# Performance work log

Hardware: AMD Instinct MI355X
Metric: run time of the kernel (lower is better)

## Reference

```python
import jax, jax.numpy as jnp
import numpy as np

NV, NC, E = 100000, 50000, 800000   # var nodes, config nodes, edges per direction
K = 100                              # configs per graph (uniform -> static dense batch)
B = NC // K                          # number of graphs
DV, DC, DH, DO = 64, 16, 128, 64     # var feat, config feat, hidden, out


def _w(key, i, o):
    # kaiming_normal_ init as in _init_weights
    return jax.random.normal(key, (i, o), jnp.float32) * np.float32(np.sqrt(2.0 / i))


def setup_inputs() -> dict:
    key = jax.random.key(0)
    ks = jax.random.split(key, 16)
    return {
        "x_var": jax.random.normal(ks[0], (NV, DV), jnp.float32),
        "x_config": jax.random.normal(ks[1], (NC, DC), jnp.float32),
        "src_v2c": jax.random.randint(ks[2], (E,), 0, NV, jnp.int32),
        "dst_v2c": jax.random.randint(ks[3], (E,), 0, NC, jnp.int32),
        "src_c2v": jax.random.randint(ks[4], (E,), 0, NC, jnp.int32),
        "dst_c2v": jax.random.randint(ks[5], (E,), 0, NV, jnp.int32),
        "batch_config": jnp.arange(NC, dtype=jnp.int32) // K,
        # layer 1 SAGEConv params per edge type (lin_l has bias, lin_r has none)
        "Wl1_v2c": _w(ks[6], DV, DH), "bl1_v2c": jnp.zeros((DH,), jnp.float32), "Wr1_v2c": _w(ks[7], DC, DH),
        "Wl1_c2v": _w(ks[8], DC, DH), "bl1_c2v": jnp.zeros((DH,), jnp.float32), "Wr1_c2v": _w(ks[9], DV, DH),
        # layer 2 (output layer, jk=None -> maps to out_channels)
        "Wl2_v2c": _w(ks[10], DH, DO), "bl2_v2c": jnp.zeros((DO,), jnp.float32), "Wr2_v2c": _w(ks[11], DH, DO),
    }


def _sage(x_src, x_dst, src, dst, Wl, bl, Wr, n_dst):
    # PyG SAGEConv: lin_l(mean_{j in N(i)} x_src[j]) + lin_r(x_dst[i])
    msum = jax.ops.segment_sum(x_src[src], dst, num_segments=n_dst)            # [n_dst, d_src]
    cnt = jax.ops.segment_sum(jnp.ones(src.shape, x_src.dtype), dst, num_segments=n_dst)
    mean = msum / jnp.maximum(cnt, 1.0)[:, None]
    return mean @ Wl + bl + x_dst @ Wr


def reference(x_var, x_config, src_v2c, dst_v2c, src_c2v, dst_c2v, batch_config,
              Wl1_v2c, bl1_v2c, Wr1_v2c, Wl1_c2v, bl1_c2v, Wr1_c2v,
              Wl2_v2c, bl2_v2c, Wr2_v2c):
    # --- layer 1 (to_hetero: each node type updated by its incoming edge type), ReLU between layers ---
    h_config = jax.nn.relu(_sage(x_var, x_config, src_v2c, dst_v2c, Wl1_v2c, bl1_v2c, Wr1_v2c, NC))
    h_var = jax.nn.relu(_sage(x_config, x_var, src_c2v, dst_c2v, Wl1_c2v, bl1_c2v, Wr1_c2v, NV))
    # --- layer 2: only the 'config' output is consumed downstream ---
    o_config = _sage(h_var, h_config, src_v2c, dst_v2c, Wl2_v2c, bl2_v2c, Wr2_v2c, NC)  # [NC, DO]
    # --- to_dense_batch(x['config'], batch) -> [B, K, DO]; squeeze() is a no-op (no size-1 dims) ---
    cnt = jax.ops.segment_sum(jnp.ones((NC,), jnp.int32), batch_config, num_segments=B)
    starts = jnp.cumsum(cnt) - cnt
    pos = jnp.arange(NC, dtype=jnp.int32) - starts[batch_config]
    dense = jnp.zeros((B, K, DO), o_config.dtype).at[batch_config, pos].set(o_config)
    return dense
```

## Files before the change

### kernel.cpp

```cpp
#include <hip/hip_runtime.h>


#define CHUNK 4096
#define EPT 16
#define MAXBINS 1024

__global__ __launch_bounds__(256) void part_count2_kernel(
    const int* __restrict__ dstC, const int* __restrict__ dstV, int E, int nblocks,
    int nbinsC, int nbinsV, int* __restrict__ countsC, int* __restrict__ countsV) {
    const int* dst; int shift, nbins; int* counts; int b;
    if (blockIdx.x < (unsigned)nblocks) { dst = dstC; shift = 6; nbins = nbinsC; counts = countsC; b = blockIdx.x; }
    else { dst = dstV; shift = 7; nbins = nbinsV; counts = countsV; b = blockIdx.x - nblocks; }
    __shared__ int hist[MAXBINS];
    int t = threadIdx.x;
    for (int j = t; j < nbins; j += 256) hist[j] = 0;
    __syncthreads();
    int base = b * CHUNK;
#pragma unroll
    for (int j = 0; j < EPT; ++j) {
        int e = base + j * 256 + t;
        if (e < E) atomicAdd(&hist[dst[e] >> shift], 1);
    }
    __syncthreads();
    for (int j = t; j < nbins; j += 256) counts[(size_t)j * nblocks + b] = hist[j];
}

__global__ __launch_bounds__(256) void part_rowscan2_kernel(
    int* __restrict__ countsC, int nbinsC, int* __restrict__ binTotC,
    int* __restrict__ countsV, int* __restrict__ binTotV, int nblocks) {
    int* counts; int* binTot; int bin;
    if (blockIdx.x < (unsigned)nbinsC) { counts = countsC; binTot = binTotC; bin = blockIdx.x; }
    else { counts = countsV; binTot = binTotV; bin = blockIdx.x - nbinsC; }
    __shared__ int s[256];
    int t = threadIdx.x;
    int v = (t < nblocks) ? counts[(size_t)bin * nblocks + t] : 0;
    s[t] = v; __syncthreads();
    for (int o = 1; o < 256; o <<= 1) {
        int add = (t >= o) ? s[t - o] : 0; __syncthreads();
        s[t] += add; __syncthreads();
    }
    if (t < nblocks) counts[(size_t)bin * nblocks + t] = s[t] - v;
    if (t == nblocks - 1) binTot[bin] = s[t];
}

__global__ __launch_bounds__(256) void part_binscan2_kernel(
    const int* __restrict__ binTotC, int nbinsC, int* __restrict__ binBaseC,
    const int* __restrict__ binTotV, int nbinsV, int* __restrict__ binBaseV) {
    const int* binTot; int nbins; int* binBase;
    if (blockIdx.x == 0) { binTot = binTotC; nbins = nbinsC; binBase = binBaseC; }
    else { binTot = binTotV; nbins = nbinsV; binBase = binBaseV; }
    __shared__ int s[256];
    __shared__ int carry;
    int t = threadIdx.x;
    if (t == 0) carry = 0;
    __syncthreads();
    for (int c0 = 0; c0 < nbins; c0 += 256) {
        int v = (c0 + t < nbins) ? binTot[c0 + t] : 0;
        s[t] = v; __syncthreads();
        for (int o = 1; o < 256; o <<= 1) {
            int add = (t >= o) ? s[t - o] : 0; __syncthreads();
            s[t] += add; __syncthreads();
        }
        if (c0 + t < nbins) binBase[c0 + t] = carry + s[t] - v;
        __syncthreads();
        if (t == 255) carry += s[255];
        __syncthreads();
    }
    if (t == 0) binBase[nbins] = carry;
}

__global__ __launch_bounds__(256) void part_scatter2_kernel(
    const int* __restrict__ srcC, const int* __restrict__ dstC,
    const int* __restrict__ srcV, const int* __restrict__ dstV, int E, int nblocks,
    int nbinsC, const int* __restrict__ countsC, const int* __restrict__ binBaseC,
    int* __restrict__ ebufC,
    int nbinsV, const int* __restrict__ countsV, const int* __restrict__ binBaseV,
    int* __restrict__ ebufV) {
    const int *src, *dst, *counts, *binBase; int* ebuf; int shift, mask, nbins; int b;
    if (blockIdx.x < (unsigned)nblocks) {
        src = srcC; dst = dstC; counts = countsC; binBase = binBaseC; ebuf = ebufC;
        shift = 6; mask = 63; nbins = nbinsC; b = blockIdx.x;
    } else {
        src = srcV; dst = dstV; counts = countsV; binBase = binBaseV; ebuf = ebufV;
        shift = 7; mask = 127; nbins = nbinsV; b = blockIdx.x - nblocks;
    }
    __shared__ int hist[MAXBINS];
    int t = threadIdx.x;
    for (int j = t; j < nbins; j += 256) hist[j] = 0;
    __syncthreads();
    int base = b * CHUNK;
#pragma unroll
    for (int j = 0; j < EPT; ++j) {
        int e = base + j * 256 + t;
        if (e < E) {
            int d = dst[e];
            int bin = d >> shift;
            int rank = atomicAdd(&hist[bin], 1);
            int slot = binBase[bin] + counts[(size_t)bin * nblocks + b] + rank;
            ebuf[slot] = (src[e] << shift) | (d & mask);
        }
    }
}

__global__ __launch_bounds__(256) void csr2_kernel(
    int nbinsC, const int* __restrict__ binBaseC, const int* __restrict__ ebufC,
    int* __restrict__ ebufC2, int* __restrict__ offC, int nC,
    const int* __restrict__ binBaseV, const int* __restrict__ ebufV,
    int* __restrict__ ebufV2, int* __restrict__ offV, int nV, int E) {
    __shared__ int hist[128];
    __shared__ int cur[128];
    __shared__ int s[256];
    int t = threadIdx.x;
    const int *binBase, *eb1; int *eb2, *off; int n, shift, bin;
    if (blockIdx.x < (unsigned)nbinsC) {
        bin = blockIdx.x; binBase = binBaseC; eb1 = ebufC; eb2 = ebufC2; off = offC; n = nC; shift = 6;
    } else {
        bin = blockIdx.x - nbinsC; binBase = binBaseV; eb1 = ebufV; eb2 = ebufV2; off = offV; n = nV; shift = 7;
    }
    int mask = (1 << shift) - 1, nloc = 1 << shift;
    if (blockIdx.x == 0 && t == 0) { offC[nC] = E; offV[nV] = E; }
    int e0 = binBase[bin], e1 = binBase[bin + 1];
    if (t < nloc) { hist[t] = 0; cur[t] = 0; }
    __syncthreads();
    for (int e = e0 + t; e < e1; e += 256) atomicAdd(&hist[eb1[e] & mask], 1);
    __syncthreads();
    int v = (t < nloc) ? hist[t] : 0;
    s[t] = v; __syncthreads();
    for (int o = 1; o < 256; o <<= 1) {
        int add = (t >= o) ? s[t - o] : 0; __syncthreads();
        s[t] += add; __syncthreads();
    }
    if (t < nloc) {
        int node = (bin << shift) + t;
        if (node < n) off[node] = e0 + s[t] - v;
        hist[t] = s[t] - v;
    }
    __syncthreads();
    for (int e = e0 + t; e < e1; e += 256) {
        int w = eb1[e];
        int local = w & mask;
        int r = atomicAdd(&cur[local], 1);
        eb2[e0 + hist[local] + r] = w >> shift;
    }
}

__device__ __forceinline__ void gather64_body(
    const int* __restrict__ off, const int* __restrict__ eb,
    const float* __restrict__ X, float* __restrict__ M,
    const float* __restrict__ P, float* __restrict__ out,
    int n, int b, int nblocks) {
    int lane = threadIdx.x & 63, wid = threadIdx.x >> 6;
    int nw = nblocks * 4;
    for (int i = b * 4 + wid; i < n; i += nw) {
        int e0 = off[i], e1 = off[i + 1];
        int deg = e1 - e0;
        float acc = 0.f;
        for (int j0 = 0; j0 < deg; j0 += 64) {
            int m = min(deg - j0, 64);
            int idx = 0;
            if (lane < m) idx = eb[e0 + j0 + lane];
            int j = 0;
            for (; j + 4 <= m; j += 4) {
                int s0 = __shfl(idx, j);
                int s1 = __shfl(idx, j + 1);
                int s2 = __shfl(idx, j + 2);
                int s3 = __shfl(idx, j + 3);
                acc += X[(size_t)s0 * 64 + lane];
                acc += X[(size_t)s1 * 64 + lane];
                acc += X[(size_t)s2 * 64 + lane];
                acc += X[(size_t)s3 * 64 + lane];
            }
            for (; j < m; ++j) {
                int s = __shfl(idx, j);
                acc += X[(size_t)s * 64 + lane];
            }
        }
        float r = acc / fmaxf((float)deg, 1.0f);
        if (out) out[(size_t)i * 64 + lane] = r + P[(size_t)i * 64 + lane];
        else     M[(size_t)i * 64 + lane] = r;
    }
}

__device__ __forceinline__ void gather16_body(
    const int* __restrict__ off, const int* __restrict__ eb,
    const float* __restrict__ X, float* __restrict__ M, int n, int b, int nblocks) {
    int lane = threadIdx.x & 63, wid = threadIdx.x >> 6;
    int dlane = lane & 15, eg = lane >> 4;
    int nw = nblocks * 4;
    for (int i = b * 4 + wid; i < n; i += nw) {
        int e0 = off[i], e1 = off[i + 1];
        int deg = e1 - e0;
        float acc = 0.f;
        for (int j0 = 0; j0 < deg; j0 += 64) {
            int m = min(deg - j0, 64);
            int idx = 0;
            if (lane < m) idx = eb[e0 + j0 + lane];
            for (int j = eg; j < m; j += 4) {
                int s = __shfl(idx, j);
                acc += X[(size_t)s * 16 + dlane];
            }
        }
        acc += __shfl_xor(acc, 16);
        acc += __shfl_xor(acc, 32);
        if (lane < 16) M[(size_t)i * 16 + lane] = acc / fmaxf((float)deg, 1.0f);
    }
}

__global__ __launch_bounds__(256) void gather2_kernel(
    const int* __restrict__ offC, const int* __restrict__ ebC,
    const float* __restrict__ Xc, float* __restrict__ Mc, int nC, int gbC,
    const int* __restrict__ offV, const int* __restrict__ ebV,
    const float* __restrict__ Xv, float* __restrict__ Mv, int nV, int gbV) {
    if (blockIdx.x < (unsigned)gbC)
        gather64_body(offC, ebC, Xc, Mc, nullptr, nullptr, nC, blockIdx.x, gbC);
    else
        gather16_body(offV, ebV, Xv, Mv, nV, blockIdx.x - gbC, gbV);
}

__global__ __launch_bounds__(256) void gather64_add_kernel(
    const int* __restrict__ off, const int* __restrict__ eb,
    const float* __restrict__ X, const float* __restrict__ P,
    float* __restrict__ out, int n) {
    gather64_body(off, eb, X, nullptr, P, out, n, blockIdx.x, gridDim.x);
}

template<int D, int ROW0>
__device__ __forceinline__ void stageF_swz(const float* __restrict__ A, float* __restrict__ Fb,
                                           int i0, int n, int t) {
    const int Q = D / 4;
    const int NPP = 256 / Q;
#pragma unroll
    for (int p = 0; p < 64 / NPP; ++p) {
        int nn = t / Q + p * NPP;
        int k4 = t % Q;
        int node = i0 + nn;
        float4 v = make_float4(0.f, 0.f, 0.f, 0.f);
        if (node < n) v = ((const float4*)A)[(size_t)node * Q + k4];
        int cs = (((nn >> 2) + (ROW0 >> 2) + k4) & 15) * 4 + (nn & 3);
        float* q = Fb + (ROW0 + 4 * k4) * 68 + cs;
        q[0 * 68] = v.x; q[1 * 68] = v.y; q[2 * 68] = v.z; q[3 * 68] = v.w;
    }
}

template<int D1, int D2, bool HASB2>
__global__ __launch_bounds__(256) void gemm_swz_kernel(
    const float* __restrict__ M, const float* __restrict__ X,
    const float* __restrict__ Wl, const float* __restrict__ Wr,
    const float* __restrict__ bias, const float* __restrict__ W2,
    const float* __restrict__ bias2, float* __restrict__ O, int n) {
    __shared__ float Fb[128 * 68];
    int t = threadIdx.x;
    int i0 = blockIdx.x * 64;
    stageF_swz<D1, 0>(M, Fb, i0, n, t);
    stageF_swz<D2, D1>(X, Fb, i0, n, t);
    __syncthreads();
    int tc = t & 15, tn = t >> 4;
    int c0 = tc * 4, n0 = tn * 4;
    float acc[4][8];
#pragma unroll
    for (int j = 0; j < 4; ++j)
#pragma unroll
        for (int jj = 0; jj < 8; ++jj) acc[j][jj] = 0.f;
#pragma unroll 4
    for (int k = 0; k < D1; ++k) {
        int sw = ((tn + (k >> 2)) & 15) * 4;
        float4 f  = *(const float4*)&Fb[k * 68 + sw];
        float4 wa = *(const float4*)&Wl[k * 128 + c0];
        float4 wc = *(const float4*)&Wl[k * 128 + 64 + c0];
        float ff[4] = {f.x, f.y, f.z, f.w};
        float va[4] = {wa.x, wa.y, wa.z, wa.w};
        float vb[4] = {wc.x, wc.y, wc.z, wc.w};
#pragma unroll
        for (int j = 0; j < 4; ++j)
#pragma unroll
            for (int jj = 0; jj < 4; ++jj) {
                acc[j][jj]     += ff[j] * va[jj];
                acc[j][4 + jj] += ff[j] * vb[jj];
            }
    }
#pragma unroll 4
    for (int k = 0; k < D2; ++k) {
        int kr = D1 + k;
        int sw = ((tn + (kr >> 2)) & 15) * 4;
        float4 f  = *(const float4*)&Fb[kr * 68 + sw];
        float4 wa = *(const float4*)&Wr[k * 128 + c0];
        float4 wc = *(const float4*)&Wr[k * 128 + 64 + c0];
        float ff[4] = {f.x, f.y, f.z, f.w};
        float va[4] = {wa.x, wa.y, wa.z, wa.w};
        float vb[4] = {wc.x, wc.y, wc.z, wc.w};
#pragma unroll
        for (int j = 0; j < 4; ++j)
#pragma unroll
            for (int jj = 0; jj < 4; ++jj) {
                acc[j][jj]     += ff[j] * va[jj];
                acc[j][4 + jj] += ff[j] * vb[jj];
            }
    }
    __syncthreads();
    {
        float4 blo = ((const float4*)bias)[tc];
        float4 bhi = ((const float4*)bias)[16 + tc];
        float bl[8] = {blo.x, blo.y, blo.z, blo.w, bhi.x, bhi.y, bhi.z, bhi.w};
        int sw1 = ((tn + tc) & 15) * 4;
        int sw2 = ((tn + 16 + tc) & 15) * 4;
#pragma unroll
        for (int jj = 0; jj < 4; ++jj) {
            float4 h1, h2;
            h1.x = fmaxf(acc[0][jj] + bl[jj], 0.f);
            h1.y = fmaxf(acc[1][jj] + bl[jj], 0.f);
            h1.z = fmaxf(acc[2][jj] + bl[jj], 0.f);
            h1.w = fmaxf(acc[3][jj] + bl[jj], 0.f);
            h2.x = fmaxf(acc[0][4 + jj] + bl[4 + jj], 0.f);
            h2.y = fmaxf(acc[1][4 + jj] + bl[4 + jj], 0.f);
            h2.z = fmaxf(acc[2][4 + jj] + bl[4 + jj], 0.f);
            h2.w = fmaxf(acc[3][4 + jj] + bl[4 + jj], 0.f);
            *(float4*)&Fb[(c0 + jj) * 68 + sw1] = h1;
            *(float4*)&Fb[(64 + c0 + jj) * 68 + sw2] = h2;
        }
    }
    __syncthreads();
    float a2[4][4];
#pragma unroll
    for (int j = 0; j < 4; ++j)
#pragma unroll
        for (int jj = 0; jj < 4; ++jj) a2[j][jj] = 0.f;
#pragma unroll 4
    for (int k = 0; k < 128; ++k) {
        int sw = ((tn + (k >> 2)) & 15) * 4;
        float4 h = *(const float4*)&Fb[k * 68 + sw];
        float4 w = *(const float4*)&W2[k * 64 + c0];
        float hh[4] = {h.x, h.y, h.z, h.w};
        float ww[4] = {w.x, w.y, w.z, w.w};
#pragma unroll
        for (int j = 0; j < 4; ++j)
#pragma unroll
            for (int jj = 0; jj < 4; ++jj) a2[j][jj] += hh[j] * ww[jj];
    }
    float4 b2 = HASB2 ? ((const float4*)bias2)[tc] : make_float4(0.f, 0.f, 0.f, 0.f);
#pragma unroll
    for (int j = 0; j < 4; ++j) {
        int node = i0 + n0 + j;
        if (node < n) {
            float4 o = {a2[j][0] + b2.x, a2[j][1] + b2.y, a2[j][2] + b2.z, a2[j][3] + b2.w};
            ((float4*)O)[(size_t)node * 16 + tc] = o;
        }
    }
}

extern "C" void kernel_launch(void* const* d_in, const int* in_sizes, int n_in,
                              void* d_out, int out_size, void* d_ws, size_t ws_size,
                              hipStream_t stream) {
    const float* x_var    = (const float*)d_in[0];
    const float* x_config = (const float*)d_in[1];
    const int* src_v2c = (const int*)d_in[2];
    const int* dst_v2c = (const int*)d_in[3];
    const int* src_c2v = (const int*)d_in[4];
    const int* dst_c2v = (const int*)d_in[5];
    const float* Wl1_v2c = (const float*)d_in[7];
    const float* bl1_v2c = (const float*)d_in[8];
    const float* Wr1_v2c = (const float*)d_in[9];
    const float* Wl1_c2v = (const float*)d_in[10];
    const float* bl1_c2v = (const float*)d_in[11];
    const float* Wr1_c2v = (const float*)d_in[12];
    const float* Wl2 = (const float*)d_in[13];
    const float* bl2 = (const float*)d_in[14];
    const float* Wr2 = (const float*)d_in[15];
    float* out = (float*)d_out;

    int NV = in_sizes[0] / 64;
    int NC = in_sizes[1] / 16;
    int E  = in_sizes[2];

    int nblocks = (E + CHUNK - 1) / CHUNK;
    int nbins_c = (NC + 63) >> 6;
    int nbins_v = (NV + 127) >> 7;

    char* p = (char*)d_ws;
    float* Mc  = (float*)p; p += (size_t)NC * 64 * 4;
    float* Mv  = (float*)p; p += (size_t)NV * 16 * 4;
    float* OCp = (float*)p; p += (size_t)NC * 64 * 4;
    float* hv2 = (float*)p; p += (size_t)NV * 64 * 4;
    int* countsC = (int*)p; p += (size_t)nbins_c * nblocks * 4;
    int* countsV = (int*)p; p += (size_t)nbins_v * nblocks * 4;
    int* binTotC = (int*)p; p += (size_t)nbins_c * 4;
    int* binTotV = (int*)p; p += (size_t)nbins_v * 4;
    int* binBaseC = (int*)p; p += (size_t)(nbins_c + 1) * 4;
    int* binBaseV = (int*)p; p += (size_t)(nbins_v + 1) * 4;
    int* offC = (int*)p; p += (size_t)(NC + 1) * 4;
    int* offV = (int*)p; p += (size_t)(NV + 1) * 4;
    int* ebufC  = (int*)p; p += (size_t)E * 4;
    int* ebufV  = (int*)p; p += (size_t)E * 4;
    int* ebufC2 = (int*)p; p += (size_t)E * 4;
    int* ebufV2 = (int*)p; p += (size_t)E * 4;

    part_count2_kernel<<<2 * nblocks, 256, 0, stream>>>(
        dst_v2c, dst_c2v, E, nblocks, nbins_c, nbins_v, countsC, countsV);
    part_rowscan2_kernel<<<nbins_c + nbins_v, 256, 0, stream>>>(
        countsC, nbins_c, binTotC, countsV, binTotV, nblocks);
    part_binscan2_kernel<<<2, 256, 0, stream>>>(
        binTotC, nbins_c, binBaseC, binTotV, nbins_v, binBaseV);
    part_scatter2_kernel<<<2 * nblocks, 256, 0, stream>>>(
        src_v2c, dst_v2c, src_c2v, dst_c2v, E, nblocks,
        nbins_c, countsC, binBaseC, ebufC,
        nbins_v, countsV, binBaseV, ebufV);
    csr2_kernel<<<nbins_c + nbins_v, 256, 0, stream>>>(
        nbins_c, binBaseC, ebufC, ebufC2, offC, NC,
        binBaseV, ebufV, ebufV2, offV, NV, E);

    int gbC = (NC + 3) / 4, gbV = (NV + 3) / 4;
    gather2_kernel<<<gbC + gbV, 256, 0, stream>>>(
        offC, ebufC2, x_var, Mc, NC, gbC,
        offV, ebufV2, x_config, Mv, NV, gbV);

    gemm_swz_kernel<64, 16, true><<<(NC + 63) / 64, 256, 0, stream>>>(
        Mc, x_config, Wl1_v2c, Wr1_v2c, bl1_v2c, Wr2, bl2, OCp, NC);
    gemm_swz_kernel<16, 64, false><<<(NV + 63) / 64, 256, 0, stream>>>(
        Mv, x_var, Wl1_c2v, Wr1_c2v, bl1_c2v, Wl2, nullptr, hv2, NV);

    gather64_add_kernel<<<gbC, 256, 0, stream>>>(offC, ebufC2, hv2, OCp, out, NC);
}
```

Before: 349.4 us.

## Stage half of GEMM weights in LDS and split second GEMM over K

Copies half of the layer-1 weights (Wl/Wr, the low 64 output columns) into a new shared buffer per block, then reuses that buffer for half of W2. The other half of each weight matrix is still read through global/L1. The second GEMM is restructured so each thread covers 8 output columns over half of K, and the two K halves are combined with a shfl_xor reduction. The aim is to cut global/L1 weight traffic and balance load sources, at the cost of more LDS use (lower occupancy), extra staging work per block, and cross-lane shuffles.

```diff
diff --git a/kernel.cpp b/kernel.cpp
--- a/kernel.cpp
+++ b/kernel.cpp
@@ -249,13 +249,22 @@
     const float* __restrict__ bias, const float* __restrict__ W2,
     const float* __restrict__ bias2, float* __restrict__ O, int n) {
     __shared__ float Fb[128 * 68];
+    __shared__ float Wb[80 * 64];
     int t = threadIdx.x;
     int i0 = blockIdx.x * 64;
+    {
+        const float4* wl4 = (const float4*)Wl;
+        const float4* wr4 = (const float4*)Wr;
+        float4* wb4 = (float4*)Wb;
+        for (int j = t; j < D1 * 16; j += 256) wb4[j] = wl4[(j >> 4) * 32 + (j & 15)];
+        for (int j = t; j < D2 * 16; j += 256) wb4[D1 * 16 + j] = wr4[(j >> 4) * 32 + (j & 15)];
+    }
     stageF_swz<D1, 0>(M, Fb, i0, n, t);
     stageF_swz<D2, D1>(X, Fb, i0, n, t);
     __syncthreads();
     int tc = t & 15, tn = t >> 4;
     int c0 = tc * 4, n0 = tn * 4;
+    const float4* wb4r = (const float4*)Wb;
     float acc[4][8];
 #pragma unroll
     for (int j = 0; j < 4; ++j)
@@ -265,8 +274,8 @@
     for (int k = 0; k < D1; ++k) {
         int sw = ((tn + (k >> 2)) & 15) * 4;
         float4 f  = *(const float4*)&Fb[k * 68 + sw];
-        float4 wa = *(const float4*)&Wl[k * 128 + c0];
-        float4 wc = *(const float4*)&Wl[k * 128 + 64 + c0];
+        float4 wa = wb4r[k * 16 + tc];
+        float4 wc = ((const float4*)Wl)[k * 32 + 16 + tc];
         float ff[4] = {f.x, f.y, f.z, f.w};
         float va[4] = {wa.x, wa.y, wa.z, wa.w};
         float vb[4] = {wc.x, wc.y, wc.z, wc.w};
@@ -283,8 +292,8 @@
         int kr = D1 + k;
         int sw = ((tn + (kr >> 2)) & 15) * 4;
         float4 f  = *(const float4*)&Fb[kr * 68 + sw];
-        float4 wa = *(const float4*)&Wr[k * 128 + c0];
-        float4 wc = *(const float4*)&Wr[k * 128 + 64 + c0];
+        float4 wa = wb4r[kr * 16 + tc];
+        float4 wc = ((const float4*)Wr)[k * 32 + 16 + tc];
         float ff[4] = {f.x, f.y, f.z, f.w};
         float va[4] = {wa.x, wa.y, wa.z, wa.w};
         float vb[4] = {wc.x, wc.y, wc.z, wc.w};
@@ -317,32 +326,53 @@
             *(float4*)&Fb[(c0 + jj) * 68 + sw1] = h1;
             *(float4*)&Fb[(64 + c0 + jj) * 68 + sw2] = h2;
         }
-    }
-    __syncthreads();
-    float a2[4][4];
+        const float4* w24 = (const float4*)W2;
+        float4* wb4 = (float4*)Wb;
+        for (int j = t; j < 128 * 8; j += 256) wb4[j] = w24[(j >> 3) * 16 + (j & 7) * 2];
+    }
+    __syncthreads();
+    int half = tc >> 3, tcc = tc & 7;
+    int kb = half * 64;
+    float a2[4][8];
 #pragma unroll
     for (int j = 0; j < 4; ++j)
 #pragma unroll
-        for (int jj = 0; jj < 4; ++jj) a2[j][jj] = 0.f;
+        for (int jj = 0; jj < 8; ++jj) a2[j][jj] = 0.f;
 #pragma unroll 4
-    for (int k = 0; k < 128; ++k) {
+    for (int kk = 0; kk < 64; ++kk) {
+        int k = kb + kk;
         int sw = ((tn + (k >> 2)) & 15) * 4;
-        float4 h = *(const float4*)&Fb[k * 68 + sw];
-        float4 w = *(const float4*)&W2[k * 64 + c0];
+        float4 h  = *(const float4*)&Fb[k * 68 + sw];
+        float4 wa = wb4r[k * 8 + tcc];
+        float4 wc = ((const float4*)W2)[k * 16 + tcc * 2 + 1];
         float hh[4] = {h.x, h.y, h.z, h.w};
-        float ww[4] = {w.x, w.y, w.z, w.w};
+        float va[4] = {wa.x, wa.y, wa.z, wa.w};
+        float vb[4] = {wc.x, wc.y, wc.z, wc.w};
 #pragma unroll
         for (int j = 0; j < 4; ++j)
 #pragma unroll
-            for (int jj = 0; jj < 4; ++jj) a2[j][jj] += hh[j] * ww[jj];
-    }
-    float4 b2 = HASB2 ? ((const float4*)bias2)[tc] : make_float4(0.f, 0.f, 0.f, 0.f);
+            for (int jj = 0; jj < 4; ++jj) {
+                a2[j][jj]     += hh[j] * va[jj];
+                a2[j][4 + jj] += hh[j] * vb[jj];
+            }
+    }
+#pragma unroll
+    for (int j = 0; j < 4; ++j)
+#pragma unroll
+        for (int jj = 0; jj < 8; ++jj)
+            a2[j][jj] += __shfl_xor(a2[j][jj], 8);
+    float4 b2 = HASB2 ? ((const float4*)bias2)[tcc * 2 + half]
+                      : make_float4(0.f, 0.f, 0.f, 0.f);
 #pragma unroll
     for (int j = 0; j < 4; ++j) {
         int node = i0 + n0 + j;
         if (node < n) {
-            float4 o = {a2[j][0] + b2.x, a2[j][1] + b2.y, a2[j][2] + b2.z, a2[j][3] + b2.w};
-            ((float4*)O)[(size_t)node * 16 + tc] = o;
+            float4 o;
+            if (half == 0)
+                o = make_float4(a2[j][0] + b2.x, a2[j][1] + b2.y, a2[j][2] + b2.z, a2[j][3] + b2.w);
+            else
+                o = make_float4(a2[j][4] + b2.x, a2[j][5] + b2.y, a2[j][6] + b2.z, a2[j][7] + b2.w);
+            ((float4*)O)[(size_t)node * 16 + tcc * 2 + half] = o;
         }
     }
 }
```

Result: no change. 354.7 us (+1.5%).
